# Performance work log

Measured on AMD Instinct MI355X. Metric: run time of the kernel, lower is better.

## Reference

```python
import jax, jax.numpy as jnp
import numpy as np

D_MODEL, N_LAYERS, D_INNER, D_STATE, D_CONV, DT_RANK, NUM_CLASSES = 256, 4, 512, 16, 4, 16, 10
B, L = 8, 1024


def setup_inputs() -> dict:
    key = jax.random.key(0)
    ks = jax.random.split(key, 16)
    s = 0.02
    inp = {}
    inp['x'] = jax.random.normal(ks[0], (B, L, 1), jnp.float32)
    inp['input_w'] = jax.random.normal(ks[1], (D_MODEL, 1), jnp.float32) * s
    inp['input_b'] = jnp.zeros((D_MODEL,), jnp.float32)
    inp['ln_w'] = jnp.ones((N_LAYERS, D_MODEL), jnp.float32)
    inp['ln_b'] = jnp.zeros((N_LAYERS, D_MODEL), jnp.float32)
    inp['in_proj_w'] = jax.random.normal(ks[2], (N_LAYERS, 2 * D_INNER, D_MODEL), jnp.float32) * s
    inp['in_proj_b'] = jnp.zeros((N_LAYERS, 2 * D_INNER), jnp.float32)
    inp['conv_w'] = jax.random.normal(ks[3], (N_LAYERS, D_INNER, 1, D_CONV), jnp.float32) * 0.2
    inp['conv_b'] = jnp.zeros((N_LAYERS, D_INNER), jnp.float32)
    inp['x_proj_w'] = jax.random.normal(ks[4], (N_LAYERS, DT_RANK + 2 * D_STATE, D_INNER), jnp.float32) * s
    inp['dt_proj_w'] = jax.random.normal(ks[5], (N_LAYERS, D_INNER, DT_RANK), jnp.float32) * s
    inp['dt_proj_b'] = jax.random.normal(ks[6], (N_LAYERS, D_INNER), jnp.float32) * 0.1 - 4.0  # small softplus(dt)
    # canonical S4D-real init: A = [1..d_state] repeated over d_inner
    A = jnp.tile(jnp.arange(1, D_STATE + 1, dtype=jnp.float32)[None, :], (D_INNER, 1))
    inp['A_log'] = jnp.tile(jnp.log(A)[None], (N_LAYERS, 1, 1))
    inp['D'] = jnp.ones((N_LAYERS, D_INNER), jnp.float32)
    inp['out_proj_w'] = jax.random.normal(ks[7], (N_LAYERS, D_MODEL, D_INNER), jnp.float32) * s
    inp['out_proj_b'] = jnp.zeros((N_LAYERS, D_MODEL), jnp.float32)
    inp['norm_w'] = jnp.ones((D_MODEL,), jnp.float32)
    inp['norm_b'] = jnp.zeros((D_MODEL,), jnp.float32)
    inp['cls_w'] = jax.random.normal(ks[8], (NUM_CLASSES, D_MODEL), jnp.float32) * s
    inp['cls_b'] = jnp.zeros((NUM_CLASSES,), jnp.float32)
    return inp


def _layernorm(x, w, b, eps=1e-5):
    mu = jnp.mean(x, axis=-1, keepdims=True)
    var = jnp.mean(jnp.square(x - mu), axis=-1, keepdims=True)
    return (x - mu) * jax.lax.rsqrt(var + eps) * w + b


def _causal_depthwise_conv(u, w, b):
    # u: (B, L, D_inner), w: (D_inner, 1, K), causal padding K-1
    out = jax.lax.conv_general_dilated(
        u.transpose(0, 2, 1), w, window_strides=(1,), padding=[(D_CONV - 1, 0)],
        feature_group_count=D_INNER, dimension_numbers=('NCH', 'OIH', 'NCH'))
    return out.transpose(0, 2, 1) + b


def _selective_scan(u, delta, A, Bm, Cm, Dp):
    # u, delta: (B,L,Din); Bm, Cm: (B,L,N); A: (Din,N); Dp: (Din,)
    def step(h, inp):
        d_t, B_t, C_t, u_t = inp                       # (B,Din),(B,N),(B,N),(B,Din)
        dA = jnp.exp(d_t[:, :, None] * A)              # (B,Din,N)
        dBu = d_t[:, :, None] * B_t[:, None, :] * u_t[:, :, None]
        h = dA * h + dBu
        y = jnp.einsum('bdn,bn->bd', h, C_t)
        return h, y
    h0 = jnp.zeros((u.shape[0], D_INNER, D_STATE), u.dtype)
    xs = (delta.transpose(1, 0, 2), Bm.transpose(1, 0, 2), Cm.transpose(1, 0, 2), u.transpose(1, 0, 2))
    _, ys = jax.lax.scan(step, h0, xs)                 # ys: (L,B,Din)
    return ys.transpose(1, 0, 2) + u * Dp


def _mamba_layer(x, ln_w, ln_b, ipw, ipb, cw, cb, xpw, dtw, dtb, A_log, Dp, opw, opb):
    h = _layernorm(x, ln_w, ln_b)
    xz = jnp.einsum('bld,ed->ble', h, ipw) + ipb       # (B,L,2*Din)
    u, res = jnp.split(xz, 2, axis=-1)
    u = jax.nn.silu(_causal_depthwise_conv(u, cw, cb))
    x_dbl = jnp.einsum('bld,ed->ble', u, xpw)          # (B,L,dt_rank+2N)
    dt, Bm, Cm = jnp.split(x_dbl, [DT_RANK, DT_RANK + D_STATE], axis=-1)
    delta = jax.nn.softplus(jnp.einsum('blr,dr->bld', dt, dtw) + dtb)
    A = -jnp.exp(A_log)
    y = _selective_scan(u, delta, A, Bm, Cm, Dp)
    y = y * jax.nn.silu(res)
    return x + jnp.einsum('ble,de->bld', y, opw) + opb


def reference(x, input_w, input_b, ln_w, ln_b, in_proj_w, in_proj_b, conv_w, conv_b,
              x_proj_w, dt_proj_w, dt_proj_b, A_log, D, out_proj_w, out_proj_b,
              norm_w, norm_b, cls_w, cls_b):
    h = jnp.einsum('blc,dc->bld', x, input_w) + input_b   # (B,L,D_MODEL)
    for i in range(N_LAYERS):
        h = _mamba_layer(h, ln_w[i], ln_b[i], in_proj_w[i], in_proj_b[i], conv_w[i], conv_b[i],
                         x_proj_w[i], dt_proj_w[i], dt_proj_b[i], A_log[i], D[i],
                         out_proj_w[i], out_proj_b[i])
    h = _layernorm(h, norm_w, norm_b)
    pooled = jnp.mean(h, axis=1)                          # (B, D_MODEL)
    return jnp.einsum('bd,cd->bc', pooled, cls_w) + cls_b
```

## Files before the change

### kernel.cpp

```cpp
#include <hip/hip_runtime.h>
#include <hip/hip_bf16.h>
#include <math.h>

#define DM 256
#define NL 4
#define DI 512
#define DS 16
#define DC 4
#define DR 16
#define NC 10
#define NB 8
#define LL 1024
#define MR (NB*LL)
#define NCHUNK 64
#define CLEN 16

typedef __attribute__((ext_vector_type(4))) float f32x4;
typedef __attribute__((ext_vector_type(8))) short short8;

extern "C" __device__ float __ocml_native_exp2_f32(float);
__device__ __forceinline__ float exp2_f(float x) { return __ocml_native_exp2_f32(x); }
#define L2E 1.442695040888963f

__device__ __forceinline__ float silu_f(float x) {
    return x * (1.0f / (1.0f + __expf(-x)));
}
__device__ __forceinline__ float bf2f(ushort v) {
    union { unsigned u; float f; } c; c.u = ((unsigned)v) << 16; return c.f;
}
__device__ __forceinline__ ushort f2bf(float f) {
    union { float f; unsigned u; } c; c.f = f;
    unsigned lsb = (c.u >> 16) & 1;
    return (ushort)((c.u + 0x7fffu + lsb) >> 16);
}
__device__ __forceinline__ void g2lds16(const void* g, void* l) {
    __builtin_amdgcn_global_load_lds((const __attribute__((address_space(1))) void*)g,
                                     (__attribute__((address_space(3))) void*)l, 16, 0, 0);
}

#define IPW_N (NL*2*DI*DM)
#define XPW_N (NL*64*DI)
#define OPW_N (NL*DM*DI)
__global__ __launch_bounds__(256) void convert_weights_kernel(
        const float* __restrict__ ipw, const float* __restrict__ xpw,
        const float* __restrict__ opw,
        ushort* __restrict__ ipw_b, ushort* __restrict__ xpw_b, ushort* __restrict__ opw_b) {
    int t = blockIdx.x * 256 + threadIdx.x;
    if (t < IPW_N) { ipw_b[t] = f2bf(ipw[t]); return; }
    t -= IPW_N;
    if (t < XPW_N) {
        int l = t >> 15, r = (t >> 9) & 63, k = t & 511;
        xpw_b[t] = (r < 48) ? f2bf(xpw[((size_t)l * 48 + r) * DI + k]) : (ushort)0;
        return;
    }
    t -= XPW_N;
    if (t < OPW_N) opw_b[t] = f2bf(opw[t]);
}

__global__ void input_proj_kernel(const float* __restrict__ x, const float* __restrict__ w,
                                  const float* __restrict__ b, float* __restrict__ h) {
    int t = blockIdx.x * 256 + threadIdx.x;
    if (t >= MR * DM) return;
    int d = t & (DM - 1);
    int m = t >> 8;
    h[t] = x[m] * w[d] + b[d];
}

__global__ __launch_bounds__(256) void layernorm_bf16_kernel(const float* __restrict__ in,
        const float* __restrict__ w, const float* __restrict__ b, ushort* __restrict__ out) {
    int row = blockIdx.x, t = threadIdx.x;
    float v = in[row * DM + t];
    float s = v, q = v * v;
#pragma unroll
    for (int o = 32; o >= 1; o >>= 1) { s += __shfl_xor(s, o); q += __shfl_xor(q, o); }
    __shared__ float red[8];
    int wid = t >> 6;
    if ((t & 63) == 0) { red[wid] = s; red[4 + wid] = q; }
    __syncthreads();
    s = red[0] + red[1] + red[2] + red[3];
    q = red[4] + red[5] + red[6] + red[7];
    float mu = s * (1.0f / DM);
    float var = q * (1.0f / DM) - mu * mu;
    float rs = rsqrtf(var + 1e-5f);
    out[row * DM + t] = f2bf((v - mu) * rs * w[t] + b[t]);
}

template<int BM, int BN, int WM, int WN, int MODE>
__global__ __launch_bounds__(256) void mfma_gemm_kernel(
        const ushort* __restrict__ A, int lda,
        const ushort* __restrict__ W,
        const float* __restrict__ bias,
        ushort* __restrict__ Cb, float* __restrict__ Cf, int ldc, int K) {
    constexpr int FM = BM / WM / 16;
    constexpr int FN = BN / WN / 16;
    __shared__ __align__(16) char smem[(BM + BN) * 128];
    const int tid = threadIdx.x;
    const int l = tid & 63, w = tid >> 6;
    const int wr = w / WN, wc = w % WN;
    const int bm = blockIdx.x * BM, bn = blockIdx.y * BN;
    const int ldw = K;

    f32x4 acc[FM][FN] = {};

    for (int k0 = 0; k0 < K; k0 += 64) {
#pragma unroll
        for (int i = 0; i < (BM * 128 / 16) / 256; i++) {
            int lin = (i * 256 + tid) * 16;
            int q = lin ^ (((lin >> 7) & 7) << 4);
            g2lds16(A + (size_t)(bm + (q >> 7)) * lda + k0 + ((q & 127) >> 1), smem + lin);
        }
#pragma unroll
        for (int i = 0; i < (BN * 128 / 16) / 256; i++) {
            int lin = (i * 256 + tid) * 16;
            int q = lin ^ (((lin >> 7) & 7) << 4);
            g2lds16(W + (size_t)(bn + (q >> 7)) * ldw + k0 + ((q & 127) >> 1),
                    smem + BM * 128 + lin);
        }
        __syncthreads();
        const int rl = l & 15;
        const int kb0 = ((l >> 4) << 3) * 2;
#pragma unroll
        for (int kk = 0; kk < 2; kk++) {
            short8 af[FM], bfr[FN];
#pragma unroll
            for (int m = 0; m < FM; m++) {
                int off = (wr * (BM / WM) + m * 16 + rl) * 128 + kk * 64 + kb0;
                off ^= ((off >> 7) & 7) << 4;
                af[m] = *(const short8*)(smem + off);
            }
#pragma unroll
            for (int n = 0; n < FN; n++) {
                int off = (wc * (BN / WN) + n * 16 + rl) * 128 + kk * 64 + kb0;
                off ^= ((off >> 7) & 7) << 4;
                bfr[n] = *(const short8*)(smem + BM * 128 + off);
            }
#pragma unroll
            for (int m = 0; m < FM; m++)
#pragma unroll
                for (int n = 0; n < FN; n++)
                    acc[m][n] = __builtin_amdgcn_mfma_f32_16x16x32_bf16(
                        af[m], bfr[n], acc[m][n], 0, 0, 0);
        }
        __syncthreads();
    }

    const int row0 = bm + wr * (BM / WM) + ((l >> 4) << 2);
    const int col0 = bn + wc * (BN / WN) + (l & 15);
#pragma unroll
    for (int m = 0; m < FM; m++) {
#pragma unroll
        for (int n = 0; n < FN; n++) {
            int col = col0 + n * 16;
            float bv = (MODE == 1) ? 0.f : bias[col];
#pragma unroll
            for (int r = 0; r < 4; r++) {
                size_t idx = (size_t)(row0 + m * 16 + r) * ldc + col;
                float v = acc[m][n][r];
                if (MODE == 0) Cb[idx] = f2bf(v + bv);
                else if (MODE == 1) Cf[idx] = v;
                else Cf[idx] += v + bv;
            }
        }
    }
}

__global__ __launch_bounds__(256) void conv_silu_kernel(const ushort* __restrict__ xz,
        const float* __restrict__ cw, const float* __restrict__ cb, ushort* __restrict__ u) {
    int t = blockIdx.x * 256 + threadIdx.x;
    int d8 = (t & 63) << 3;
    int m = t >> 6;
    int l = m & (LL - 1);
    const short8 zr = {0, 0, 0, 0, 0, 0, 0, 0};
    const size_t base = (size_t)m * 1024 + d8;
    short8 r3 = *(const short8*)(xz + base);
    short8 r2 = (l >= 1) ? *(const short8*)(xz + base - 1024) : zr;
    short8 r1 = (l >= 2) ? *(const short8*)(xz + base - 2048) : zr;
    short8 r0 = (l >= 3) ? *(const short8*)(xz + base - 3072) : zr;
    short8 o;
#pragma unroll
    for (int j = 0; j < 8; j++) {
        int d = d8 + j;
        float4 w4 = *reinterpret_cast<const float4*>(&cw[d * 4]);
        float a = cb[d] + w4.w * bf2f((ushort)r3[j]);
        a += w4.z * bf2f((ushort)r2[j]);
        a += w4.y * bf2f((ushort)r1[j]);
        a += w4.x * bf2f((ushort)r0[j]);
        o[j] = (short)f2bf(silu_f(a));
    }
    *(short8*)(u + (size_t)m * DI + d8) = o;
}

__global__ __launch_bounds__(256, 4) void scan_phase1_kernel(
        const ushort* __restrict__ u, const float* __restrict__ x_dbl,
        const float* __restrict__ A_log,
        const float* __restrict__ dtw, const float* __restrict__ dtb,
        float* __restrict__ sdv, float* __restrict__ Sbuf) {
    __shared__ __align__(16) float xs[CLEN * 64];
    const int tid = threadIdx.x;
    const int bc = blockIdx.x >> 1;
    const int d = ((blockIdx.x & 1) << 8) + tid;
    const int c = bc & (NCHUNK - 1);
    const int b = bc >> 6;
    const int m0 = b * LL + c * CLEN;
    *reinterpret_cast<float4*>(&xs[tid * 4]) =
        *reinterpret_cast<const float4*>(&x_dbl[(size_t)m0 * 64 + tid * 4]);

    float Aval[DS], h[DS], wreg[DR];
#pragma unroll
    for (int q = 0; q < 4; q++) {
        float4 a4 = *reinterpret_cast<const float4*>(&A_log[d * DS + q * 4]);
        Aval[q*4+0] = -__expf(a4.x) * L2E; Aval[q*4+1] = -__expf(a4.y) * L2E;
        Aval[q*4+2] = -__expf(a4.z) * L2E; Aval[q*4+3] = -__expf(a4.w) * L2E;
        float4 w4 = *reinterpret_cast<const float4*>(&dtw[d * DR + q * 4]);
        wreg[q*4] = w4.x; wreg[q*4+1] = w4.y; wreg[q*4+2] = w4.z; wreg[q*4+3] = w4.w;
    }
    float dbv = dtb[d];
#pragma unroll
    for (int n = 0; n < DS; n++) h[n] = 0.f;
    const ushort* up = u + (size_t)m0 * DI + d;
    float sd = 0.f;
    __syncthreads();
    float uv = bf2f(up[0]);
    for (int t = 0; t < CLEN; t++) {
        float uvn = (t + 1 < CLEN) ? bf2f(up[(size_t)(t + 1) * DI]) : 0.f;
        const float* xr = &xs[t * 64];
        float4 x0 = *reinterpret_cast<const float4*>(xr);
        float4 x1 = *reinterpret_cast<const float4*>(xr + 4);
        float4 x2 = *reinterpret_cast<const float4*>(xr + 8);
        float4 x3 = *reinterpret_cast<const float4*>(xr + 12);
        float4 B0 = *reinterpret_cast<const float4*>(xr + 16);
        float4 B1 = *reinterpret_cast<const float4*>(xr + 20);
        float4 B2 = *reinterpret_cast<const float4*>(xr + 24);
        float4 B3 = *reinterpret_cast<const float4*>(xr + 28);
        float p0 = dbv + wreg[0]*x0.x + wreg[1]*x0.y + wreg[2]*x0.z + wreg[3]*x0.w;
        float p1 = wreg[4]*x1.x + wreg[5]*x1.y + wreg[6]*x1.z + wreg[7]*x1.w;
        float p2 = wreg[8]*x2.x + wreg[9]*x2.y + wreg[10]*x2.z + wreg[11]*x2.w;
        float p3 = wreg[12]*x3.x + wreg[13]*x3.y + wreg[14]*x3.z + wreg[15]*x3.w;
        float z = (p0 + p1) + (p2 + p3);
        float dv = (z > 20.0f) ? z : __logf(1.0f + __expf(z));
        sd += dv;
        float du = dv * uv;
        h[0]  = exp2_f(dv*Aval[0])  * h[0]  + du * B0.x;
        h[1]  = exp2_f(dv*Aval[1])  * h[1]  + du * B0.y;
        h[2]  = exp2_f(dv*Aval[2])  * h[2]  + du * B0.z;
        h[3]  = exp2_f(dv*Aval[3])  * h[3]  + du * B0.w;
        h[4]  = exp2_f(dv*Aval[4])  * h[4]  + du * B1.x;
        h[5]  = exp2_f(dv*Aval[5])  * h[5]  + du * B1.y;
        h[6]  = exp2_f(dv*Aval[6])  * h[6]  + du * B1.z;
        h[7]  = exp2_f(dv*Aval[7])  * h[7]  + du * B1.w;
        h[8]  = exp2_f(dv*Aval[8])  * h[8]  + du * B2.x;
        h[9]  = exp2_f(dv*Aval[9])  * h[9]  + du * B2.y;
        h[10] = exp2_f(dv*Aval[10]) * h[10] + du * B2.z;
        h[11] = exp2_f(dv*Aval[11]) * h[11] + du * B2.w;
        h[12] = exp2_f(dv*Aval[12]) * h[12] + du * B3.x;
        h[13] = exp2_f(dv*Aval[13]) * h[13] + du * B3.y;
        h[14] = exp2_f(dv*Aval[14]) * h[14] + du * B3.z;
        h[15] = exp2_f(dv*Aval[15]) * h[15] + du * B3.w;
        uv = uvn;
    }
    size_t base = ((size_t)((b * NCHUNK + c) * DI + d)) * DS;
#pragma unroll
    for (int q = 0; q < 4; q++)
        *reinterpret_cast<float4*>(&Sbuf[base + q * 4]) =
            make_float4(h[q*4], h[q*4+1], h[q*4+2], h[q*4+3]);
    sdv[(b * NCHUNK + c) * DI + d] = sd;
}

__global__ __launch_bounds__(256) void scan_phase2_kernel(
        const float* __restrict__ sdv, const float* __restrict__ A_log,
        float* __restrict__ Sbuf) {
    int gid = blockIdx.x * 256 + threadIdx.x;
    int dn = gid & (DI * DS - 1);
    int b = gid >> 13;
    int n = dn & 15, d = dn >> 4;
    float Aval = -__expf(A_log[d * DS + n]) * L2E;
    size_t idx0 = (size_t)b * NCHUNK * DI * DS + dn;
    const size_t stride = (size_t)DI * DS;
    int sb0 = b * NCHUNK * DI + d;
    float h = 0.f;
    float Sc = Sbuf[idx0];
    float sd = sdv[sb0];
    for (int c = 0; c < NCHUNK; c++) {
        size_t idx = idx0 + (size_t)c * stride;
        float Sn = 0.f, sdn = 0.f;
        if (c + 1 < NCHUNK) {
            Sn = Sbuf[idx + stride];
            sdn = sdv[sb0 + (c + 1) * DI];
        }
        float Pc = exp2_f(Aval * sd);
        Sbuf[idx] = h;
        h = Pc * h + Sc;
        Sc = Sn; sd = sdn;
    }
}

__global__ __launch_bounds__(256, 4) void scan_phase3_kernel(
        const ushort* __restrict__ u, const float* __restrict__ x_dbl,
        const float* __restrict__ A_log,
        const float* __restrict__ dtw, const float* __restrict__ dtb,
        const float* __restrict__ Dp, const float* __restrict__ Sbuf,
        const ushort* __restrict__ xz, ushort* __restrict__ y) {
    __shared__ __align__(16) float xs[CLEN * 64];
    const int tid = threadIdx.x;
    const int bc = blockIdx.x >> 1;
    const int d = ((blockIdx.x & 1) << 8) + tid;
    const int c = bc & (NCHUNK - 1);
    const int b = bc >> 6;
    const int m0 = b * LL + c * CLEN;
    *reinterpret_cast<float4*>(&xs[tid * 4]) =
        *reinterpret_cast<const float4*>(&x_dbl[(size_t)m0 * 64 + tid * 4]);

    float Aval[DS], h[DS], wreg[DR];
#pragma unroll
    for (int q = 0; q < 4; q++) {
        float4 a4 = *reinterpret_cast<const float4*>(&A_log[d * DS + q * 4]);
        Aval[q*4+0] = -__expf(a4.x) * L2E; Aval[q*4+1] = -__expf(a4.y) * L2E;
        Aval[q*4+2] = -__expf(a4.z) * L2E; Aval[q*4+3] = -__expf(a4.w) * L2E;
        float4 w4 = *reinterpret_cast<const float4*>(&dtw[d * DR + q * 4]);
        wreg[q*4] = w4.x; wreg[q*4+1] = w4.y; wreg[q*4+2] = w4.z; wreg[q*4+3] = w4.w;
    }
    float dbv = dtb[d];
    size_t base = ((size_t)((b * NCHUNK + c) * DI + d)) * DS;
#pragma unroll
    for (int q = 0; q < 4; q++) {
        float4 h4 = *reinterpret_cast<const float4*>(&Sbuf[base + q * 4]);
        h[q*4] = h4.x; h[q*4+1] = h4.y; h[q*4+2] = h4.z; h[q*4+3] = h4.w;
    }
    float Dval = Dp[d];
    const ushort* up = u + (size_t)m0 * DI + d;
    const ushort* rp = xz + (size_t)m0 * 1024 + 512 + d;
    ushort* yp = y + (size_t)m0 * DI + d;
    __syncthreads();
    float uv = bf2f(up[0]);
    float rv = bf2f(rp[0]);
    for (int t = 0; t < CLEN; t++) {
        float uvn = 0.f, rvn = 0.f;
        if (t + 1 < CLEN) {
            uvn = bf2f(up[(size_t)(t + 1) * DI]);
            rvn = bf2f(rp[(size_t)(t + 1) * 1024]);
        }
        const float* xr = &xs[t * 64];
        float4 x0 = *reinterpret_cast<const float4*>(xr);
        float4 x1 = *reinterpret_cast<const float4*>(xr + 4);
        float4 x2 = *reinterpret_cast<const float4*>(xr + 8);
        float4 x3 = *reinterpret_cast<const float4*>(xr + 12);
        float4 B0 = *reinterpret_cast<const float4*>(xr + 16);
        float4 B1 = *reinterpret_cast<const float4*>(xr + 20);
        float4 B2 = *reinterpret_cast<const float4*>(xr + 24);
        float4 B3 = *reinterpret_cast<const float4*>(xr + 28);
        float4 C0 = *reinterpret_cast<const float4*>(xr + 32);
        float4 C1 = *reinterpret_cast<const float4*>(xr + 36);
        float4 C2 = *reinterpret_cast<const float4*>(xr + 40);
        float4 C3 = *reinterpret_cast<const float4*>(xr + 44);
        float p0 = dbv + wreg[0]*x0.x + wreg[1]*x0.y + wreg[2]*x0.z + wreg[3]*x0.w;
        float p1 = wreg[4]*x1.x + wreg[5]*x1.y + wreg[6]*x1.z + wreg[7]*x1.w;
        float p2 = wreg[8]*x2.x + wreg[9]*x2.y + wreg[10]*x2.z + wreg[11]*x2.w;
        float p3 = wreg[12]*x3.x + wreg[13]*x3.y + wreg[14]*x3.z + wreg[15]*x3.w;
        float z = (p0 + p1) + (p2 + p3);
        float dv = (z > 20.0f) ? z : __logf(1.0f + __expf(z));
        float du = dv * uv;
        float a0, a1, a2, a3;
        h[0]  = exp2_f(dv*Aval[0])  * h[0]  + du * B0.x;  a0  = h[0]  * C0.x;
        h[1]  = exp2_f(dv*Aval[1])  * h[1]  + du * B0.y;  a0 += h[1]  * C0.y;
        h[2]  = exp2_f(dv*Aval[2])  * h[2]  + du * B0.z;  a0 += h[2]  * C0.z;
        h[3]  = exp2_f(dv*Aval[3])  * h[3]  + du * B0.w;  a0 += h[3]  * C0.w;
        h[4]  = exp2_f(dv*Aval[4])  * h[4]  + du * B1.x;  a1  = h[4]  * C1.x;
        h[5]  = exp2_f(dv*Aval[5])  * h[5]  + du * B1.y;  a1 += h[5]  * C1.y;
        h[6]  = exp2_f(dv*Aval[6])  * h[6]  + du * B1.z;  a1 += h[6]  * C1.z;
        h[7]  = exp2_f(dv*Aval[7])  * h[7]  + du * B1.w;  a1 += h[7]  * C1.w;
        h[8]  = exp2_f(dv*Aval[8])  * h[8]  + du * B2.x;  a2  = h[8]  * C2.x;
        h[9]  = exp2_f(dv*Aval[9])  * h[9]  + du * B2.y;  a2 += h[9]  * C2.y;
        h[10] = exp2_f(dv*Aval[10]) * h[10] + du * B2.z;  a2 += h[10] * C2.z;
        h[11] = exp2_f(dv*Aval[11]) * h[11] + du * B2.w;  a2 += h[11] * C2.w;
        h[12] = exp2_f(dv*Aval[12]) * h[12] + du * B3.x;  a3  = h[12] * C3.x;
        h[13] = exp2_f(dv*Aval[13]) * h[13] + du * B3.y;  a3 += h[13] * C3.y;
        h[14] = exp2_f(dv*Aval[14]) * h[14] + du * B3.z;  a3 += h[14] * C3.z;
        h[15] = exp2_f(dv*Aval[15]) * h[15] + du * B3.w;  a3 += h[15] * C3.w;
        float acc = ((a0 + a1) + (a2 + a3)) + Dval * uv;
        yp[(size_t)t * DI] = f2bf(acc * silu_f(rv));
        uv = uvn; rv = rvn;
    }
}

__global__ __launch_bounds__(256) void pool_partial_kernel(const ushort* __restrict__ ln,
                                                           float* __restrict__ partial) {
    int bs = blockIdx.x;
    int b = bs >> 3, sl = bs & 7;
    int t = threadIdx.x;
    int l0 = sl * 128;
    float s = 0.f;
    for (int l = 0; l < 128; l++) s += bf2f(ln[(size_t)(b * LL + l0 + l) * DM + t]);
    partial[(bs << 8) + t] = s;
}

__global__ void cls_kernel(const float* __restrict__ partial, const float* __restrict__ cw,
                           const float* __restrict__ cb, float* __restrict__ out) {
    int t = threadIdx.x;
    if (t >= NB * NC) return;
    int b = t / NC, c = t % NC;
    float s = 0.f;
    for (int k = 0; k < DM; k++) {
        float p = 0.f;
#pragma unroll
        for (int sl = 0; sl < 8; sl++) p += partial[((b * 8 + sl) << 8) + k];
        s += p * cw[c * DM + k];
    }
    out[t] = cb[c] + s * (1.0f / LL);
}

extern "C" void kernel_launch(void* const* d_in, const int* in_sizes, int n_in,
                              void* d_out, int out_size, void* d_ws, size_t ws_size,
                              hipStream_t stream) {
    const float* x       = (const float*)d_in[0];
    const float* input_w = (const float*)d_in[1];
    const float* input_b = (const float*)d_in[2];
    const float* ln_w    = (const float*)d_in[3];
    const float* ln_b    = (const float*)d_in[4];
    const float* ipw     = (const float*)d_in[5];
    const float* ipb     = (const float*)d_in[6];
    const float* cw      = (const float*)d_in[7];
    const float* cb      = (const float*)d_in[8];
    const float* xpw     = (const float*)d_in[9];
    const float* dtw     = (const float*)d_in[10];
    const float* dtb     = (const float*)d_in[11];
    const float* A_log   = (const float*)d_in[12];
    const float* Dp      = (const float*)d_in[13];
    const float* opw     = (const float*)d_in[14];
    const float* opb     = (const float*)d_in[15];
    const float* norm_w  = (const float*)d_in[16];
    const float* norm_b  = (const float*)d_in[17];
    const float* cls_w   = (const float*)d_in[18];
    const float* cls_b   = (const float*)d_in[19];
    float* out = (float*)d_out;
    float* ws = (float*)d_ws;

    float*  hres   = ws;
    ushort* xz     = (ushort*)(hres + (size_t)MR * DM);
    ushort* ub     = xz + (size_t)MR * 1024;
    float*  x_dbl  = (float*)(ub + (size_t)MR * DI);
    float*  sdvb   = x_dbl + (size_t)MR * 64;
    float*  Sbuf   = sdvb + (size_t)NB * NCHUNK * DI;
    float*  partial= Sbuf + (size_t)NB * NCHUNK * DI * DS;
    ushort* ygate  = (ushort*)(partial + 64 * 256);
    ushort* hln    = ygate + (size_t)MR * DI;
    ushort* ipw_b  = hln + (size_t)MR * DM;
    ushort* xpw_b  = ipw_b + IPW_N;
    ushort* opw_b  = xpw_b + XPW_N;

    convert_weights_kernel<<<(IPW_N + XPW_N + OPW_N) / 256, 256, 0, stream>>>(
        ipw, xpw, opw, ipw_b, xpw_b, opw_b);
    input_proj_kernel<<<MR * DM / 256, 256, 0, stream>>>(x, input_w, input_b, hres);

    for (int i = 0; i < NL; i++) {
        layernorm_bf16_kernel<<<MR, 256, 0, stream>>>(hres, ln_w + i * DM, ln_b + i * DM, hln);
        mfma_gemm_kernel<128, 128, 2, 2, 0><<<dim3(MR / 128, 1024 / 128), 256, 0, stream>>>(
            hln, DM, ipw_b + (size_t)i * 2 * DI * DM, ipb + (size_t)i * 2 * DI,
            xz, nullptr, 1024, DM);
        conv_silu_kernel<<<MR * DI / 8 / 256, 256, 0, stream>>>(xz, cw + i * DI * DC, cb + i * DI, ub);
        mfma_gemm_kernel<64, 64, 4, 1, 1><<<dim3(MR / 64, 1), 256, 0, stream>>>(
            ub, DI, xpw_b + (size_t)i * 64 * DI, nullptr, nullptr, x_dbl, 64, DI);
        scan_phase1_kernel<<<NB * NCHUNK * DI / 256, 256, 0, stream>>>(
            ub, x_dbl, A_log + i * DI * DS, dtw + i * DI * DR, dtb + i * DI, sdvb, Sbuf);
        scan_phase2_kernel<<<NB * DI * DS / 256, 256, 0, stream>>>(
            sdvb, A_log + i * DI * DS, Sbuf);
        scan_phase3_kernel<<<NB * NCHUNK * DI / 256, 256, 0, stream>>>(
            ub, x_dbl, A_log + i * DI * DS, dtw + i * DI * DR, dtb + i * DI,
            Dp + i * DI, Sbuf, xz, ygate);
        mfma_gemm_kernel<64, 128, 2, 2, 2><<<dim3(MR / 64, DM / 128), 256, 0, stream>>>(
            ygate, DI, opw_b + (size_t)i * DM * DI, opb + (size_t)i * DM,
            nullptr, hres, DM, DI);
    }

    layernorm_bf16_kernel<<<MR, 256, 0, stream>>>(hres, norm_w, norm_b, hln);
    pool_partial_kernel<<<64, 256, 0, stream>>>(hln, partial);
    cls_kernel<<<1, 128, 0, stream>>>(partial, cls_w, cls_b, out);
}
```

Baseline: 486.4 us.

## Fuse out-projection residual add with next layer's LayerNorm; batch scan phase2 loads

Replaces the out-projection GEMM and the separate LayerNorm launch with one kernel. Each block covers 32 full rows across all 256 columns, adds bias and residual, writes hres, then computes the row statistics for the next layer's (or the final) LayerNorm and writes the bf16 normalized activations. This removes a launch and a full read of hres per layer, at the cost of a smaller grid (256 blocks) and the single-pass variance formula. Scan phase 2 also now prefetches eight chunks of S and sd at a time to hide memory latency in the sequential loop.

```diff
diff --git a/kernel.cpp b/kernel.cpp
--- a/kernel.cpp
+++ b/kernel.cpp
@@ -157,8 +157,135 @@
                 size_t idx = (size_t)(row0 + m * 16 + r) * ldc + col;
                 float v = acc[m][n][r];
                 if (MODE == 0) Cb[idx] = f2bf(v + bv);
-                else if (MODE == 1) Cf[idx] = v;
-                else Cf[idx] += v + bv;
+                else Cf[idx] = v;
+            }
+        }
+    }
+}
+
+__global__ __launch_bounds__(256) void outproj_ln_kernel(
+        const ushort* __restrict__ A,
+        const ushort* __restrict__ W,
+        const float* __restrict__ bias,
+        float* __restrict__ hres,
+        const float* __restrict__ lnw, const float* __restrict__ lnb,
+        ushort* __restrict__ hln) {
+    constexpr int K = DI;
+    __shared__ __align__(16) char smem[(32 + 256) * 128];
+    const int tid = threadIdx.x;
+    const int l = tid & 63, w = tid >> 6;
+    const int bm = blockIdx.x * 32;
+
+    f32x4 acc[2][4] = {};
+
+    for (int k0 = 0; k0 < K; k0 += 64) {
+        {
+            int lin = tid * 16;
+            int q = lin ^ (((lin >> 7) & 7) << 4);
+            g2lds16(A + (size_t)(bm + (q >> 7)) * K + k0 + ((q & 127) >> 1), smem + lin);
+        }
+#pragma unroll
+        for (int i = 0; i < 8; i++) {
+            int lin = (i * 256 + tid) * 16;
+            int q = lin ^ (((lin >> 7) & 7) << 4);
+            g2lds16(W + (size_t)(q >> 7) * K + k0 + ((q & 127) >> 1), smem + 32 * 128 + lin);
+        }
+        __syncthreads();
+        const int rl = l & 15;
+        const int kb0 = ((l >> 4) << 3) * 2;
+#pragma unroll
+        for (int kk = 0; kk < 2; kk++) {
+            short8 af[2], bfr[4];
+#pragma unroll
+            for (int m = 0; m < 2; m++) {
+                int off = (m * 16 + rl) * 128 + kk * 64 + kb0;
+                off ^= ((off >> 7) & 7) << 4;
+                af[m] = *(const short8*)(smem + off);
+            }
+#pragma unroll
+            for (int n = 0; n < 4; n++) {
+                int off = (w * 64 + n * 16 + rl) * 128 + kk * 64 + kb0;
+                off ^= ((off >> 7) & 7) << 4;
+                bfr[n] = *(const short8*)(smem + 32 * 128 + off);
+            }
+#pragma unroll
+            for (int m = 0; m < 2; m++)
+#pragma unroll
+                for (int n = 0; n < 4; n++)
+                    acc[m][n] = __builtin_amdgcn_mfma_f32_16x16x32_bf16(
+                        af[m], bfr[n], acc[m][n], 0, 0, 0);
+        }
+        __syncthreads();
+    }
+
+    const int r0 = (l >> 4) << 2;
+    const int col0 = w * 64 + (l & 15);
+    float vv[2][4][4];
+    float s[2][4], q[2][4];
+#pragma unroll
+    for (int m = 0; m < 2; m++)
+#pragma unroll
+        for (int r = 0; r < 4; r++) { s[m][r] = 0.f; q[m][r] = 0.f; }
+#pragma unroll
+    for (int m = 0; m < 2; m++) {
+#pragma unroll
+        for (int n = 0; n < 4; n++) {
+            int col = col0 + n * 16;
+            float bv = bias[col];
+#pragma unroll
+            for (int r = 0; r < 4; r++) {
+                int row = bm + r0 + m * 16 + r;
+                float x = acc[m][n][r] + bv + hres[(size_t)row * DM + col];
+                vv[m][n][r] = x;
+                s[m][r] += x;
+                q[m][r] += x * x;
+            }
+        }
+    }
+#pragma unroll
+    for (int o = 1; o < 16; o <<= 1) {
+#pragma unroll
+        for (int m = 0; m < 2; m++)
+#pragma unroll
+            for (int r = 0; r < 4; r++) {
+                s[m][r] += __shfl_xor(s[m][r], o);
+                q[m][r] += __shfl_xor(q[m][r], o);
+            }
+    }
+    float* red  = (float*)smem;
+    float* redq = red + 128;
+    if ((l & 15) == 0) {
+#pragma unroll
+        for (int m = 0; m < 2; m++)
+#pragma unroll
+            for (int r = 0; r < 4; r++) {
+                int rl2 = r0 + m * 16 + r;
+                red[rl2 * 4 + w] = s[m][r];
+                redq[rl2 * 4 + w] = q[m][r];
+            }
+    }
+    __syncthreads();
+#pragma unroll
+    for (int m = 0; m < 2; m++) {
+        float mu[4], rs[4];
+#pragma unroll
+        for (int r = 0; r < 4; r++) {
+            int rl2 = r0 + m * 16 + r;
+            float ts = red[rl2 * 4] + red[rl2 * 4 + 1] + red[rl2 * 4 + 2] + red[rl2 * 4 + 3];
+            float tq = redq[rl2 * 4] + redq[rl2 * 4 + 1] + redq[rl2 * 4 + 2] + redq[rl2 * 4 + 3];
+            mu[r] = ts * (1.0f / DM);
+            float var = tq * (1.0f / DM) - mu[r] * mu[r];
+            rs[r] = rsqrtf(var + 1e-5f);
+        }
+#pragma unroll
+        for (int n = 0; n < 4; n++) {
+            int col = col0 + n * 16;
+            float lw = lnw[col], lb = lnb[col];
+#pragma unroll
+            for (int r = 0; r < 4; r++) {
+                int row = bm + r0 + m * 16 + r;
+                hres[(size_t)row * DM + col] = vv[m][n][r];
+                hln[(size_t)row * DM + col] = f2bf((vv[m][n][r] - mu[r]) * rs[r] * lw + lb);
             }
         }
     }
@@ -278,19 +405,33 @@
     const size_t stride = (size_t)DI * DS;
     int sb0 = b * NCHUNK * DI + d;
     float h = 0.f;
-    float Sc = Sbuf[idx0];
-    float sd = sdv[sb0];
-    for (int c = 0; c < NCHUNK; c++) {
-        size_t idx = idx0 + (size_t)c * stride;
-        float Sn = 0.f, sdn = 0.f;
-        if (c + 1 < NCHUNK) {
-            Sn = Sbuf[idx + stride];
-            sdn = sdv[sb0 + (c + 1) * DI];
-        }
-        float Pc = exp2_f(Aval * sd);
-        Sbuf[idx] = h;
-        h = Pc * h + Sc;
-        Sc = Sn; sd = sdn;
+    float S0[8], sd0[8];
+#pragma unroll
+    for (int j = 0; j < 8; j++) {
+        S0[j] = Sbuf[idx0 + (size_t)j * stride];
+        sd0[j] = sdv[sb0 + j * DI];
+    }
+    for (int g = 0; g < 8; g++) {
+        float S1[8], sd1[8];
+        if (g < 7) {
+            int c1 = g * 8 + 8;
+#pragma unroll
+            for (int j = 0; j < 8; j++) {
+                S1[j] = Sbuf[idx0 + (size_t)(c1 + j) * stride];
+                sd1[j] = sdv[sb0 + (c1 + j) * DI];
+            }
+        } else {
+#pragma unroll
+            for (int j = 0; j < 8; j++) { S1[j] = 0.f; sd1[j] = 0.f; }
+        }
+#pragma unroll
+        for (int j = 0; j < 8; j++) {
+            float P = exp2_f(Aval * sd0[j]);
+            Sbuf[idx0 + (size_t)(g * 8 + j) * stride] = h;
+            h = P * h + S0[j];
+        }
+#pragma unroll
+        for (int j = 0; j < 8; j++) { S0[j] = S1[j]; sd0[j] = sd1[j]; }
     }
 }
 
@@ -450,9 +591,9 @@
     convert_weights_kernel<<<(IPW_N + XPW_N + OPW_N) / 256, 256, 0, stream>>>(
         ipw, xpw, opw, ipw_b, xpw_b, opw_b);
     input_proj_kernel<<<MR * DM / 256, 256, 0, stream>>>(x, input_w, input_b, hres);
+    layernorm_bf16_kernel<<<MR, 256, 0, stream>>>(hres, ln_w, ln_b, hln);
 
     for (int i = 0; i < NL; i++) {
-        layernorm_bf16_kernel<<<MR, 256, 0, stream>>>(hres, ln_w + i * DM, ln_b + i * DM, hln);
         mfma_gemm_kernel<128, 128, 2, 2, 0><<<dim3(MR / 128, 1024 / 128), 256, 0, stream>>>(
             hln, DM, ipw_b + (size_t)i * 2 * DI * DM, ipb + (size_t)i * 2 * DI,
             xz, nullptr, 1024, DM);
@@ -466,12 +607,13 @@
         scan_phase3_kernel<<<NB * NCHUNK * DI / 256, 256, 0, stream>>>(
             ub, x_dbl, A_log + i * DI * DS, dtw + i * DI * DR, dtb + i * DI,
             Dp + i * DI, Sbuf, xz, ygate);
-        mfma_gemm_kernel<64, 128, 2, 2, 2><<<dim3(MR / 64, DM / 128), 256, 0, stream>>>(
-            ygate, DI, opw_b + (size_t)i * DM * DI, opb + (size_t)i * DM,
-            nullptr, hres, DM, DI);
-    }
-
-    layernorm_bf16_kernel<<<MR, 256, 0, stream>>>(hres, norm_w, norm_b, hln);
+        const float* nlw = (i < NL - 1) ? (ln_w + (i + 1) * DM) : norm_w;
+        const float* nlb = (i < NL - 1) ? (ln_b + (i + 1) * DM) : norm_b;
+        outproj_ln_kernel<<<MR / 32, 256, 0, stream>>>(
+            ygate, opw_b + (size_t)i * DM * DI, opb + (size_t)i * DM,
+            hres, nlw, nlb, hln);
+    }
+
     pool_partial_kernel<<<64, 256, 0, stream>>>(hln, partial);
     cls_kernel<<<1, 128, 0, stream>>>(partial, cls_w, cls_b, out);
 }
```

Result: faster. 444.3 us (-8.6%).
